# Optimization experiments

Measured on AMD Instinct MI355X. Metric: run time of the kernel, lower is better.

Reference implementation:

```python
import jax, jax.numpy as jnp
import numpy as np

N = 8192
IN_F = 256
OUT_F = 128
E = 262144
ALPHA = 0.2  # LeakyReLU negative slope
NEG_INF = -9e15


def setup_inputs() -> dict:
    key = jax.random.key(0)
    k_h, k_e, k_w, k_bl, k_a, k_ba = jax.random.split(key, 6)
    h = jax.random.normal(k_h, (N, IN_F), dtype=jnp.float32)
    edge_index = jax.random.randint(k_e, (2, E), 0, N, dtype=jnp.int64)
    # nn.Linear(in_features, out_features): weight [out, in], bias [out]
    lim_w = 1.0 / np.sqrt(IN_F)
    W = jax.random.uniform(k_w, (OUT_F, IN_F), minval=-lim_w, maxval=lim_w, dtype=jnp.float32)
    b_lin = jax.random.uniform(k_bl, (OUT_F,), minval=-lim_w, maxval=lim_w, dtype=jnp.float32)
    # nn.Linear(2*out_features, 1): weight [1, 2*out], bias [1]
    lim_a = 1.0 / np.sqrt(2 * OUT_F)
    a = jax.random.uniform(k_a, (1, 2 * OUT_F), minval=-lim_a, maxval=lim_a, dtype=jnp.float32)
    b_att = jax.random.uniform(k_ba, (1,), minval=-lim_a, maxval=lim_a, dtype=jnp.float32)
    return {"h": h, "edge_index": edge_index, "W": W, "b_lin": b_lin, "a": a, "b_att": b_att}


def reference(h, edge_index, W, b_lin, a, b_att):
    n = h.shape[0]
    Wh = h @ W.T + b_lin  # [N, F_out]
    # a . [Wh_i || Wh_j] + b == Wh_i.a1 + Wh_j.a2 + b  (exact decomposition of the
    # concat-pairwise attention linear; avoids materializing [N, N, 2F])
    a1 = a[0, :OUT_F]
    a2 = a[0, OUT_F:]
    s1 = Wh @ a1  # [N]
    s2 = Wh @ a2  # [N]
    e = jax.nn.leaky_relu(s1[:, None] + s2[None, :] + b_att[0], negative_slope=ALPHA)  # [N, N]
    # dense adjacency mask from edge_index (to_dense_adj semantics)
    adj = jnp.zeros((n, n), dtype=jnp.float32).at[edge_index[0], edge_index[1]].set(1.0)
    attention = jnp.where(adj > 0, e, jnp.float32(NEG_INF))
    attention = jax.nn.softmax(attention, axis=1)
    h_prime = attention @ Wh  # [N, F_out]
    return jax.nn.elu(h_prime)
```

## Files before the change

### kernel.cpp

```cpp
#include <hip/hip_runtime.h>
#include <hip/hip_bf16.h>
#include <math.h>

#define N_NODES 8192
#define IN_FEAT 256
#define OUT_FEAT 128
#define NUM_E 262144
#define LRELU_ALPHA 0.2f
#define CAP 128
#define BM_W 256

typedef __bf16 bf16x8 __attribute__((ext_vector_type(8)));
typedef float f32x4 __attribute__((ext_vector_type(4)));

__global__ __launch_bounds__(256) void k_gemm(const float* __restrict__ h,
                                              const float* __restrict__ W,
                                              const float* __restrict__ b_lin,
                                              const float* __restrict__ a_att,
                                              const float* __restrict__ b_att,
                                              __hip_bfloat16* __restrict__ Whb,
                                              float* __restrict__ s1,
                                              float* __restrict__ s2,
                                              int* __restrict__ deg) {
    const int tid = threadIdx.x;
    if (tid < 16) deg[blockIdx.x * 16 + tid] = 0;

    const int lane = tid & 63;
    const int w    = tid >> 6;
    const int m    = lane & 15;
    const int quad = lane >> 4;
    const int r0   = blockIdx.x * 16;
    const int wcol = w * 32;

    f32x4 acc[2] = {};

    const float* hrow = h + (r0 + m) * IN_FEAT + quad * 8;
    #pragma unroll
    for (int ks = 0; ks < 8; ++ks) {
        const int k = ks * 32;
        float4 ha = *(const float4*)(hrow + k);
        float4 hb = *(const float4*)(hrow + k + 4);
        bf16x8 af;
        af[0] = (__bf16)ha.x; af[1] = (__bf16)ha.y; af[2] = (__bf16)ha.z; af[3] = (__bf16)ha.w;
        af[4] = (__bf16)hb.x; af[5] = (__bf16)hb.y; af[6] = (__bf16)hb.z; af[7] = (__bf16)hb.w;
        #pragma unroll
        for (int nt = 0; nt < 2; ++nt) {
            const float* wp = W + (wcol + nt * 16 + m) * IN_FEAT + quad * 8 + k;
            float4 wa = *(const float4*)(wp);
            float4 wb = *(const float4*)(wp + 4);
            bf16x8 bfv;
            bfv[0] = (__bf16)wa.x; bfv[1] = (__bf16)wa.y; bfv[2] = (__bf16)wa.z; bfv[3] = (__bf16)wa.w;
            bfv[4] = (__bf16)wb.x; bfv[5] = (__bf16)wb.y; bfv[6] = (__bf16)wb.z; bfv[7] = (__bf16)wb.w;
            acc[nt] = __builtin_amdgcn_mfma_f32_16x16x32_bf16(af, bfv, acc[nt], 0, 0, 0);
        }
    }

    float p1[4] = {0.f, 0.f, 0.f, 0.f};
    float p2[4] = {0.f, 0.f, 0.f, 0.f};
    #pragma unroll
    for (int nt = 0; nt < 2; ++nt) {
        const int col = wcol + nt * 16 + m;
        const float bl = b_lin[col];
        const float a1 = a_att[col];
        const float a2 = a_att[OUT_FEAT + col];
        #pragma unroll
        for (int reg = 0; reg < 4; ++reg) {
            const float v = acc[nt][reg] + bl;
            const int row = r0 + quad * 4 + reg;
            Whb[row * OUT_FEAT + col] = __float2bfloat16(v);
            p1[reg] = fmaf(v, a1, p1[reg]);
            p2[reg] = fmaf(v, a2, p2[reg]);
        }
    }
    #pragma unroll
    for (int off = 1; off < 16; off <<= 1) {
        #pragma unroll
        for (int reg = 0; reg < 4; ++reg) {
            p1[reg] += __shfl_xor(p1[reg], off, 64);
            p2[reg] += __shfl_xor(p2[reg], off, 64);
        }
    }
    __shared__ float red1[16][4];
    __shared__ float red2[16][4];
    if (m == 0) {
        #pragma unroll
        for (int reg = 0; reg < 4; ++reg) {
            red1[quad * 4 + reg][w] = p1[reg];
            red2[quad * 4 + reg][w] = p2[reg];
        }
    }
    __syncthreads();
    if (tid < 16) {
        s1[r0 + tid] = red1[tid][0] + red1[tid][1] + red1[tid][2] + red1[tid][3] + b_att[0];
    } else if (tid >= 64 && tid < 80) {
        const int r = tid - 64;
        s2[r0 + r] = red2[r][0] + red2[r][1] + red2[r][2] + red2[r][3];
    }
}

__global__ __launch_bounds__(256) void k_scatter(const int* __restrict__ ei,
                                                 int* __restrict__ deg,
                                                 int* __restrict__ elist) {
    const int k4 = (blockIdx.x * 256 + threadIdx.x) * 4;
    if (k4 >= NUM_E) return;
    const int4 r = *(const int4*)&ei[k4];
    const int4 c = *(const int4*)&ei[NUM_E + k4];
    int p;
    p = atomicAdd(&deg[r.x], 1); if (p < CAP) elist[r.x * CAP + p] = c.x;
    p = atomicAdd(&deg[r.y], 1); if (p < CAP) elist[r.y * CAP + p] = c.y;
    p = atomicAdd(&deg[r.z], 1); if (p < CAP) elist[r.z * CAP + p] = c.z;
    p = atomicAdd(&deg[r.w], 1); if (p < CAP) elist[r.w * CAP + p] = c.w;
}

__global__ __launch_bounds__(128) void k_aggr(const int* __restrict__ deg,
                                              const int* __restrict__ elist,
                                              const float* __restrict__ s1,
                                              const float* __restrict__ s2,
                                              const __hip_bfloat16* __restrict__ Whb,
                                              float* __restrict__ out) {
    __shared__ unsigned int bm[BM_W];
    __shared__ float el[CAP];
    __shared__ int   jl[CAP];
    __shared__ float colred[4][128];
    __shared__ float dred[4];
    const int tid = threadIdx.x;
    const int w = tid >> 6, lane = tid & 63;
    const int i = blockIdx.x;

    const int jraw = elist[i * CAP + tid];
    const int nr   = deg[i];
    const float s1i = s1[i];
    bm[tid] = 0u; bm[tid + 128] = 0u;
    __syncthreads();
    const int n = nr < CAP ? nr : CAP;

    if (tid < n) {
        float wt = 0.f;
        jl[tid] = jraw;
        const unsigned int bit = 1u << (jraw & 31);
        const unsigned int old = atomicOr(&bm[jraw >> 5], bit);
        if (!(old & bit)) {
            float v = s1i + s2[jraw];
            v = v > 0.f ? v : LRELU_ALPHA * v;
            wt = __expf(v);
        }
        el[tid] = wt;
    }
    __syncthreads();

    const int half = lane >> 5;
    const int slot = w * 2 + half;
    const int cb = (lane & 31) * 4;
    float a0 = 0.f, a1 = 0.f, a2 = 0.f, a3 = 0.f, ds = 0.f;
    for (int t = slot; t < n; t += 4) {
        const float wv = el[t];
        const int j = jl[t];
        const uint2 u = *(const uint2*)&Whb[j * OUT_FEAT + cb];
        union { unsigned int ui; float f; } c0, c1, c2, c3;
        c0.ui = u.x << 16; c1.ui = u.x & 0xffff0000u;
        c2.ui = u.y << 16; c3.ui = u.y & 0xffff0000u;
        a0 = fmaf(wv, c0.f, a0);
        a1 = fmaf(wv, c1.f, a1);
        a2 = fmaf(wv, c2.f, a2);
        a3 = fmaf(wv, c3.f, a3);
        ds += wv;
    }
    colred[slot][cb]     = a0;
    colred[slot][cb + 1] = a1;
    colred[slot][cb + 2] = a2;
    colred[slot][cb + 3] = a3;
    if ((lane & 31) == 0) dred[slot] = ds;
    __syncthreads();

    float o;
    if (n > 0) {
        const float denom = dred[0] + dred[1] + dred[2] + dred[3];
        o = (colred[0][tid] + colred[1][tid] + colred[2][tid] + colred[3][tid]) / denom;
    } else {
        float acc = 0.f;
        for (int r = 0; r < N_NODES; ++r) acc += __bfloat162float(Whb[r * OUT_FEAT + tid]);
        o = acc * (1.f / (float)N_NODES);
    }
    out[i * OUT_FEAT + tid] = o > 0.f ? o : expm1f(o);
}

extern "C" void kernel_launch(void* const* d_in, const int* in_sizes, int n_in,
                              void* d_out, int out_size, void* d_ws, size_t ws_size,
                              hipStream_t stream) {
    const float* h     = (const float*)d_in[0];
    const int*   ei    = (const int*)d_in[1];
    const float* W     = (const float*)d_in[2];
    const float* b_lin = (const float*)d_in[3];
    const float* a     = (const float*)d_in[4];
    const float* b_att = (const float*)d_in[5];
    float* out = (float*)d_out;

    char* ws = (char*)d_ws;
    __hip_bfloat16* Whb = (__hip_bfloat16*)(ws);
    float* s1    = (float*)(ws + 2097152);
    float* s2    = (float*)(ws + 2097152 + 32768);
    int*   elist = (int*)(ws + 2097152 + 65536);
    int*   deg   = (int*)(ws + 2097152 + 65536 + 4194304);

    k_gemm<<<N_NODES / 16, 256, 0, stream>>>(h, W, b_lin, a, b_att, Whb, s1, s2, deg);
    k_scatter<<<NUM_E / 1024, 256, 0, stream>>>(ei, deg, elist);
    k_aggr<<<N_NODES, 128, 0, stream>>>(deg, elist, s1, s2, Whb, out);
}
```

Before: 102.4 us.

## Fuse edge scatter into GEMM kernel and software-pipeline the aggregation loads

Merges the edge-scatter kernel into the GEMM kernel: each block reads 512 edges and does the atomic inserts, so one launch is removed and the scatter overlaps the MFMA work. Degree zeroing moves to a hipMemsetAsync, because the blocks now write each other's counters. In the aggregation kernel the s2 gather is hoisted ahead of the barrier using a masked index, and the neighbour-row loop now loads the next row before accumulating the current one to hide latency. The cost is an extra memset operation and more atomic pressure sitting inside the GEMM kernel.

```diff
diff --git a/kernel.cpp b/kernel.cpp
--- a/kernel.cpp
+++ b/kernel.cpp
@@ -13,17 +13,22 @@
 typedef __bf16 bf16x8 __attribute__((ext_vector_type(8)));
 typedef float f32x4 __attribute__((ext_vector_type(4)));
 
-__global__ __launch_bounds__(256) void k_gemm(const float* __restrict__ h,
-                                              const float* __restrict__ W,
-                                              const float* __restrict__ b_lin,
-                                              const float* __restrict__ a_att,
-                                              const float* __restrict__ b_att,
-                                              __hip_bfloat16* __restrict__ Whb,
-                                              float* __restrict__ s1,
-                                              float* __restrict__ s2,
-                                              int* __restrict__ deg) {
+__global__ __launch_bounds__(256) void k_gemm_scatter(const float* __restrict__ h,
+                                                      const float* __restrict__ W,
+                                                      const float* __restrict__ b_lin,
+                                                      const float* __restrict__ a_att,
+                                                      const float* __restrict__ b_att,
+                                                      const int* __restrict__ ei,
+                                                      __hip_bfloat16* __restrict__ Whb,
+                                                      float* __restrict__ s1,
+                                                      float* __restrict__ s2,
+                                                      int* __restrict__ deg,
+                                                      int* __restrict__ elist) {
     const int tid = threadIdx.x;
-    if (tid < 16) deg[blockIdx.x * 16 + tid] = 0;
+
+    const int e0 = blockIdx.x * 512 + tid * 2;
+    const int2 er = *(const int2*)&ei[e0];
+    const int2 ec = *(const int2*)&ei[NUM_E + e0];
 
     const int lane = tid & 63;
     const int w    = tid >> 6;
@@ -55,6 +60,12 @@
         }
     }
 
+    {
+        int p;
+        p = atomicAdd(&deg[er.x], 1); if (p < CAP) elist[er.x * CAP + p] = ec.x;
+        p = atomicAdd(&deg[er.y], 1); if (p < CAP) elist[er.y * CAP + p] = ec.y;
+    }
+
     float p1[4] = {0.f, 0.f, 0.f, 0.f};
     float p2[4] = {0.f, 0.f, 0.f, 0.f};
     #pragma unroll
@@ -96,20 +107,6 @@
         const int r = tid - 64;
         s2[r0 + r] = red2[r][0] + red2[r][1] + red2[r][2] + red2[r][3];
     }
-}
-
-__global__ __launch_bounds__(256) void k_scatter(const int* __restrict__ ei,
-                                                 int* __restrict__ deg,
-                                                 int* __restrict__ elist) {
-    const int k4 = (blockIdx.x * 256 + threadIdx.x) * 4;
-    if (k4 >= NUM_E) return;
-    const int4 r = *(const int4*)&ei[k4];
-    const int4 c = *(const int4*)&ei[NUM_E + k4];
-    int p;
-    p = atomicAdd(&deg[r.x], 1); if (p < CAP) elist[r.x * CAP + p] = c.x;
-    p = atomicAdd(&deg[r.y], 1); if (p < CAP) elist[r.y * CAP + p] = c.y;
-    p = atomicAdd(&deg[r.z], 1); if (p < CAP) elist[r.z * CAP + p] = c.z;
-    p = atomicAdd(&deg[r.w], 1); if (p < CAP) elist[r.w * CAP + p] = c.w;
 }
 
 __global__ __launch_bounds__(128) void k_aggr(const int* __restrict__ deg,
@@ -130,6 +127,7 @@
     const int jraw = elist[i * CAP + tid];
     const int nr   = deg[i];
     const float s1i = s1[i];
+    const float s2p = s2[jraw & (N_NODES - 1)];
     bm[tid] = 0u; bm[tid + 128] = 0u;
     __syncthreads();
     const int n = nr < CAP ? nr : CAP;
@@ -140,7 +138,7 @@
         const unsigned int bit = 1u << (jraw & 31);
         const unsigned int old = atomicOr(&bm[jraw >> 5], bit);
         if (!(old & bit)) {
-            float v = s1i + s2[jraw];
+            float v = s1i + s2p;
             v = v > 0.f ? v : LRELU_ALPHA * v;
             wt = __expf(v);
         }
@@ -152,10 +150,25 @@
     const int slot = w * 2 + half;
     const int cb = (lane & 31) * 4;
     float a0 = 0.f, a1 = 0.f, a2 = 0.f, a3 = 0.f, ds = 0.f;
-    for (int t = slot; t < n; t += 4) {
-        const float wv = el[t];
-        const int j = jl[t];
-        const uint2 u = *(const uint2*)&Whb[j * OUT_FEAT + cb];
+    int t = slot;
+    if (t < n) {
+        float wv = el[t];
+        int j = jl[t];
+        uint2 u = *(const uint2*)&Whb[j * OUT_FEAT + cb];
+        for (t += 4; t < n; t += 4) {
+            const float wvn = el[t];
+            const int jn = jl[t];
+            const uint2 un = *(const uint2*)&Whb[jn * OUT_FEAT + cb];
+            union { unsigned int ui; float f; } c0, c1, c2, c3;
+            c0.ui = u.x << 16; c1.ui = u.x & 0xffff0000u;
+            c2.ui = u.y << 16; c3.ui = u.y & 0xffff0000u;
+            a0 = fmaf(wv, c0.f, a0);
+            a1 = fmaf(wv, c1.f, a1);
+            a2 = fmaf(wv, c2.f, a2);
+            a3 = fmaf(wv, c3.f, a3);
+            ds += wv;
+            wv = wvn; u = un;
+        }
         union { unsigned int ui; float f; } c0, c1, c2, c3;
         c0.ui = u.x << 16; c1.ui = u.x & 0xffff0000u;
         c2.ui = u.y << 16; c3.ui = u.y & 0xffff0000u;
@@ -202,7 +215,8 @@
     int*   elist = (int*)(ws + 2097152 + 65536);
     int*   deg   = (int*)(ws + 2097152 + 65536 + 4194304);
 
-    k_gemm<<<N_NODES / 16, 256, 0, stream>>>(h, W, b_lin, a, b_att, Whb, s1, s2, deg);
-    k_scatter<<<NUM_E / 1024, 256, 0, stream>>>(ei, deg, elist);
+    hipMemsetAsync(deg, 0, N_NODES * sizeof(int), stream);
+    k_gemm_scatter<<<N_NODES / 16, 256, 0, stream>>>(h, W, b_lin, a, b_att, ei,
+                                                     Whb, s1, s2, deg, elist);
     k_aggr<<<N_NODES, 128, 0, stream>>>(deg, elist, s1, s2, Whb, out);
 }
```

Result: no change. 101.2 us (-1.2%).
